# Kernel tuning notes

Hardware: AMD Instinct MI355X
Metric: run time of the kernel (lower is better)

Reference implementation:

```python
import jax, jax.numpy as jnp
import numpy as np


def setup_inputs() -> dict:
    key = jax.random.key(0)
    ks = jax.random.split(key, 8)
    B, C, H, W = 8, 256, 64, 64
    Ck = C // 8
    s = 0.02
    return {
        "x": jax.random.normal(ks[0], (B, C, H, W), dtype=jnp.float32),
        "Wk": jax.random.normal(ks[1], (Ck, C), dtype=jnp.float32) * s,
        "bk": jnp.zeros((Ck,), dtype=jnp.float32),
        "Wq": jax.random.normal(ks[2], (Ck, C), dtype=jnp.float32) * s,
        "bq": jnp.zeros((Ck,), dtype=jnp.float32),
        "Wv": jax.random.normal(ks[3], (C, C), dtype=jnp.float32) * s,
        "bv": jnp.zeros((C,), dtype=jnp.float32),
        "gamma": jnp.zeros((1,), dtype=jnp.float32),
    }


def reference(x, Wk, bk, Wq, bq, Wv, bv, gamma):
    B, C, H, W = x.shape
    x_flat = x.reshape(B, C, H * W)  # [B, C, N]
    # 1x1 conv1d == pointwise linear over channels
    k = jnp.einsum('oc,bcn->bon', Wk, x_flat) + bk[None, :, None]  # [B, C/8, N]
    q = jnp.einsum('oc,bcn->bon', Wq, x_flat) + bq[None, :, None]  # [B, C/8, N]
    v = jnp.einsum('oc,bcn->bon', Wv, x_flat) + bv[None, :, None]  # [B, C, N]
    affinity = jnp.einsum('bki,bkj->bij', q, k)  # [B, N, N]
    # NOTE: original computes F.softmax(affinity, dim=1) but never uses it
    # (dead code); output uses the raw affinity, reproduced faithfully here.
    out = jnp.einsum('bci,bih->bch', v, affinity).reshape(B, C, H, W)
    return gamma[0] * out + x
```

## Files before the change

### kernel.cpp

```cpp
#include <hip/hip_runtime.h>


constexpr int NB = 8;
constexpr int NC = 256;
constexpr int NK = 32;
constexpr int NN = 4096;
constexpr int NCHUNK = 64;

typedef float  f32x4  __attribute__((ext_vector_type(4)));
typedef __bf16 bf16x4 __attribute__((ext_vector_type(4)));
typedef __bf16 bf16x8 __attribute__((ext_vector_type(8)));

__device__ __forceinline__ bf16x8 load_bf8(const float* __restrict__ p) {
  f32x4 a = *(const f32x4*)p;
  f32x4 b = *(const f32x4*)(p + 4);
  bf16x8 r;
  r[0] = (__bf16)a[0]; r[1] = (__bf16)a[1]; r[2] = (__bf16)a[2]; r[3] = (__bf16)a[3];
  r[4] = (__bf16)b[0]; r[5] = (__bf16)b[1]; r[6] = (__bf16)b[2]; r[7] = (__bf16)b[3];
  return r;
}

__global__ __launch_bounds__(256) void k_front(
    const float* __restrict__ x, const float* __restrict__ Wq,
    const float* __restrict__ bq, const float* __restrict__ Wk,
    __bf16* __restrict__ Tpart, __bf16* __restrict__ Kt_t,
    float* __restrict__ qsum_part) {
  __shared__ __bf16 ldsT[64 * 264];
  __shared__ __bf16 ldsW[2][32][264];
  __shared__ __bf16 ldsQt[32][72];
  __shared__ __bf16 ldsKt[32][72];
  __shared__ float  ldsQs[4][32];
  int bid = blockIdx.x;
  int b = bid >> 6, chunk = bid & 63;
  int nsub = chunk * 64;
  int t = threadIdx.x;
  int lane = t & 63, w = t >> 6, lr = lane & 15, lg = lane >> 4;
  const float* xb = x + (size_t)b * NC * NN;
  float bq0 = bq[lr], bq1 = bq[16 + lr];

  {
    int m = t >> 7, tid = t & 127;
    int j = tid >> 2, c0 = (tid & 3) * 64;
    const float* Ws = m ? Wk : Wq;
#pragma unroll
    for (int i = 0; i < 16; ++i) {
      f32x4 v = *(const f32x4*)(Ws + j * NC + c0 + i * 4);
      bf16x4 pk = {(__bf16)v[0], (__bf16)v[1], (__bf16)v[2], (__bf16)v[3]};
      *(bf16x4*)&ldsW[m][j][c0 + i * 4] = pk;
    }
  }
  {
    int cg = t >> 4, ng = t & 15;
    int n0 = ng * 4;
    int swzEl = (ng & 7) << 3;
#pragma unroll
    for (int r = 0; r < 4; ++r) {
      int c0 = r * 64 + cg * 4;
      const float* src = xb + (size_t)c0 * NN + nsub + n0;
      f32x4 L0 = *(const f32x4*)(src);
      f32x4 L1 = *(const f32x4*)(src + NN);
      f32x4 L2 = *(const f32x4*)(src + 2 * NN);
      f32x4 L3 = *(const f32x4*)(src + 3 * NN);
#pragma unroll
      for (int jj = 0; jj < 4; ++jj) {
        bf16x4 pk = {(__bf16)L0[jj], (__bf16)L1[jj], (__bf16)L2[jj], (__bf16)L3[jj]};
        *(bf16x4*)&ldsT[(n0 + jj) * 264 + (c0 ^ swzEl)] = pk;
      }
    }
  }
  __syncthreads();
  f32x4 aq[2] = {}, ak[2] = {};
  {
    int n = w * 16 + lr;
    int swzA = ((n >> 2) & 7) << 3;
    int rowA = n * 264;
#pragma unroll
    for (int ks = 0; ks < 8; ++ks) {
      bf16x8 af = *(const bf16x8*)&ldsT[rowA + ((ks * 32 + lg * 8) ^ swzA)];
      bf16x8 q0 = *(const bf16x8*)&ldsW[0][lr][ks * 32 + lg * 8];
      bf16x8 q1 = *(const bf16x8*)&ldsW[0][16 + lr][ks * 32 + lg * 8];
      bf16x8 k0 = *(const bf16x8*)&ldsW[1][lr][ks * 32 + lg * 8];
      bf16x8 k1 = *(const bf16x8*)&ldsW[1][16 + lr][ks * 32 + lg * 8];
      aq[0] = __builtin_amdgcn_mfma_f32_16x16x32_bf16(af, q0, aq[0], 0, 0, 0);
      aq[1] = __builtin_amdgcn_mfma_f32_16x16x32_bf16(af, q1, aq[1], 0, 0, 0);
      ak[0] = __builtin_amdgcn_mfma_f32_16x16x32_bf16(af, k0, ak[0], 0, 0, 0);
      ak[1] = __builtin_amdgcn_mfma_f32_16x16x32_bf16(af, k1, ak[1], 0, 0, 0);
    }
  }
  float qs0, qs1;
#pragma unroll
  for (int r = 0; r < 4; ++r) { aq[0][r] += bq0; aq[1][r] += bq1; }
  qs0 = aq[0][0] + aq[0][1] + aq[0][2] + aq[0][3];
  qs1 = aq[1][0] + aq[1][1] + aq[1][2] + aq[1][3];
  {
    bf16x4 p0 = {(__bf16)aq[0][0], (__bf16)aq[0][1], (__bf16)aq[0][2], (__bf16)aq[0][3]};
    bf16x4 p1 = {(__bf16)aq[1][0], (__bf16)aq[1][1], (__bf16)aq[1][2], (__bf16)aq[1][3]};
    *(bf16x4*)&ldsQt[lr][w * 16 + lg * 4] = p0;
    *(bf16x4*)&ldsQt[16 + lr][w * 16 + lg * 4] = p1;
    bf16x4 k0p = {(__bf16)ak[0][0], (__bf16)ak[0][1], (__bf16)ak[0][2], (__bf16)ak[0][3]};
    bf16x4 k1p = {(__bf16)ak[1][0], (__bf16)ak[1][1], (__bf16)ak[1][2], (__bf16)ak[1][3]};
    *(bf16x4*)&ldsKt[lr][w * 16 + lg * 4] = k0p;
    *(bf16x4*)&ldsKt[16 + lr][w * 16 + lg * 4] = k1p;
  }
  __syncthreads();
  {
    int nloc = t >> 2, j0 = (t & 3) * 8;
    bf16x8 pk;
#pragma unroll
    for (int i = 0; i < 8; ++i) pk[i] = ldsKt[j0 + i][nloc];
    *(bf16x8*)&Kt_t[((size_t)b * NN + nsub + nloc) * NK + j0] = pk;
  }
  f32x4 accT[4][2] = {};
#pragma unroll
  for (int ks2 = 0; ks2 < 2; ++ks2) {
    bf16x8 bf0 = *(const bf16x8*)&ldsQt[lr][ks2 * 32 + lg * 8];
    bf16x8 bf1 = *(const bf16x8*)&ldsQt[16 + lr][ks2 * 32 + lg * 8];
#pragma unroll
    for (int mt = 0; mt < 4; ++mt) {
      int c = w * 64 + mt * 16 + lr;
      bf16x8 af = load_bf8(xb + (size_t)c * NN + nsub + ks2 * 32 + lg * 8);
      accT[mt][0] = __builtin_amdgcn_mfma_f32_16x16x32_bf16(af, bf0, accT[mt][0], 0, 0, 0);
      accT[mt][1] = __builtin_amdgcn_mfma_f32_16x16x32_bf16(af, bf1, accT[mt][1], 0, 0, 0);
    }
  }
  qs0 += __shfl_xor(qs0, 16); qs0 += __shfl_xor(qs0, 32);
  qs1 += __shfl_xor(qs1, 16); qs1 += __shfl_xor(qs1, 32);
  if (lane < 16) { ldsQs[w][lane] = qs0; ldsQs[w][16 + lane] = qs1; }
  __syncthreads();
  if (t < 32)
    qsum_part[(size_t)(chunk * NB + b) * NK + t] =
        ldsQs[0][t] + ldsQs[1][t] + ldsQs[2][t] + ldsQs[3][t];
  __bf16* Tp = Tpart + (size_t)(chunk * NB + b) * NC * NK;
#pragma unroll
  for (int mt = 0; mt < 4; ++mt)
#pragma unroll
    for (int jf = 0; jf < 2; ++jf) {
      bf16x4 pk = {(__bf16)accT[mt][jf][0], (__bf16)accT[mt][jf][1],
                   (__bf16)accT[mt][jf][2], (__bf16)accT[mt][jf][3]};
      *(bf16x4*)&Tp[(jf * 16 + lr) * NC + w * 64 + mt * 16 + lg * 4] = pk;
    }
}

__global__ __launch_bounds__(256) void k_reduce(__bf16* __restrict__ Tpart) {
  int bid = blockIdx.x;
  int b = bid >> 3, slice = bid & 7;
  int t = threadIdx.x;
  int jo = t >> 6, c0 = (t & 63) * 4;
  const size_t chstride = (size_t)NB * NK * NC;
  size_t idx = ((size_t)b * NK + slice * 4 + jo) * NC + c0;
  float acc[4] = {};
#pragma unroll 8
  for (int ch = 0; ch < NCHUNK; ++ch) {
    bf16x4 v = *(const bf16x4*)&Tpart[ch * chstride + idx];
#pragma unroll
    for (int i = 0; i < 4; ++i) acc[i] += (float)v[i];
  }
  bf16x4 o = {(__bf16)acc[0], (__bf16)acc[1], (__bf16)acc[2], (__bf16)acc[3]};
  *(bf16x4*)&Tpart[idx] = o;
}

__global__ __launch_bounds__(256) void k_pgemm(
    const __bf16* __restrict__ T, const float* __restrict__ qsum_part,
    const float* __restrict__ Wv, const float* __restrict__ bv,
    const float* __restrict__ bk, __bf16* __restrict__ P,
    float* __restrict__ h2) {
  __shared__ __bf16 shTt[16][264];
  __shared__ float shQsum[16];
  int bid = blockIdx.x;
  int b = bid >> 1, jg = bid & 1;
  int t = threadIdx.x;
  if (t < 16) {
    float s = 0.f;
#pragma unroll 8
    for (int ch = 0; ch < NCHUNK; ++ch)
      s += qsum_part[(size_t)(ch * NB + b) * NK + jg * 16 + t];
    shQsum[t] = s;
  }
  {
    int j = t >> 5, c0 = (t & 31) * 8;
    bf16x8 v = *(const bf16x8*)&T[((size_t)b * NK + jg * 16 + j) * NC + c0];
    *(bf16x8*)&shTt[j][c0] = v;
  }
  __syncthreads();
  int lane = t & 63, w = t >> 6, lr = lane & 15, lg = lane >> 4;
  float bkj = bk[jg * 16 + lr];
  f32x4 accP[4] = {};
#pragma unroll
  for (int ks = 0; ks < 8; ++ks) {
    bf16x8 b0 = *(const bf16x8*)&shTt[lr][ks * 32 + lg * 8];
#pragma unroll
    for (int mt = 0; mt < 4; ++mt) {
      int c = w * 64 + mt * 16 + lr;
      bf16x8 af = load_bf8(Wv + (size_t)c * NC + ks * 32 + lg * 8);
      accP[mt] = __builtin_amdgcn_mfma_f32_16x16x32_bf16(af, b0, accP[mt], 0, 0, 0);
    }
  }
  float qs = shQsum[lr];
#pragma unroll
  for (int mt = 0; mt < 4; ++mt) {
    float hacc[4];
#pragma unroll
    for (int r = 0; r < 4; ++r) {
      int c = w * 64 + mt * 16 + lg * 4 + r;
      float val = accP[mt][r] + bv[c] * qs;
      P[((size_t)b * NC + c) * NK + jg * 16 + lr] = (__bf16)val;
      hacc[r] = val * bkj;
    }
#pragma unroll
    for (int r = 0; r < 4; ++r) {
      float v = hacc[r];
      v += __shfl_xor(v, 1); v += __shfl_xor(v, 2);
      v += __shfl_xor(v, 4); v += __shfl_xor(v, 8);
      if (lr == 0)
        h2[((size_t)b * 2 + jg) * NC + w * 64 + mt * 16 + lg * 4 + r] = v;
    }
  }
}

__global__ __launch_bounds__(256) void k_back(
    const float* __restrict__ x, const __bf16* __restrict__ Kt_t,
    const __bf16* __restrict__ P, const float* __restrict__ h2,
    const float* __restrict__ gamma, float* __restrict__ out) {
  int bid = blockIdx.x;
  int b = bid >> 6, n0 = (bid & 63) * 64;
  int t = threadIdx.x;
  int lane = t & 63, w = t >> 6, lr = lane & 15, lg = lane >> 4;

  bf16x8 af = *(const bf16x8*)&Kt_t[((size_t)b * NN + n0 + w * 16 + lr) * NK + lg * 8];
  const __bf16* Pb = P + (size_t)b * NC * NK;
  f32x4 acc[16];
#pragma unroll
  for (int ft = 0; ft < 16; ++ft) {
    bf16x8 bfr = *(const bf16x8*)&Pb[(size_t)(ft * 16 + lr) * NK + lg * 8];
    f32x4 z = {0.f, 0.f, 0.f, 0.f};
    acc[ft] = __builtin_amdgcn_mfma_f32_16x16x32_bf16(af, bfr, z, 0, 0, 0);
  }
  float g = gamma[0];
  const float* h0 = h2 + (size_t)b * 2 * NC;
#pragma unroll
  for (int ft = 0; ft < 16; ++ft) {
    int c = ft * 16 + lr;
    float hc = h0[c] + h0[NC + c];
    size_t idx = ((size_t)b * NC + c) * NN + n0 + w * 16 + lg * 4;
    f32x4 xv = *(const f32x4*)&x[idx];
    f32x4 o;
#pragma unroll
    for (int r = 0; r < 4; ++r) o[r] = g * (acc[ft][r] + hc) + xv[r];
    *(f32x4*)&out[idx] = o;
  }
}

extern "C" void kernel_launch(void* const* d_in, const int* in_sizes, int n_in,
                              void* d_out, int out_size, void* d_ws, size_t ws_size,
                              hipStream_t stream) {
  (void)in_sizes; (void)n_in; (void)out_size; (void)ws_size;
  const float* x     = (const float*)d_in[0];
  const float* Wk    = (const float*)d_in[1];
  const float* bk    = (const float*)d_in[2];
  const float* Wq    = (const float*)d_in[3];
  const float* bq    = (const float*)d_in[4];
  const float* Wv    = (const float*)d_in[5];
  const float* bv    = (const float*)d_in[6];
  const float* gamma = (const float*)d_in[7];
  float* out = (float*)d_out;

  char* wsb = (char*)d_ws;
  const size_t tpB = (size_t)NCHUNK * NB * NC * NK * 2;
  const size_t ktB = (size_t)NB * NN * NK * 2;
  const size_t qsB = (size_t)NCHUNK * NB * NK * 4;
  const size_t pB  = (size_t)NB * NC * NK * 2;
  __bf16* Tpart = (__bf16*)wsb;
  __bf16* Kt_t  = (__bf16*)(wsb + tpB);
  float*  qsp   = (float*)(wsb + tpB + ktB);
  __bf16* P     = (__bf16*)(wsb + tpB + ktB + qsB);
  float*  h2    = (float*)(wsb + tpB + ktB + qsB + pB);

  k_front<<<NB * NCHUNK, 256, 0, stream>>>(x, Wq, bq, Wk, Tpart, Kt_t, qsp);
  k_reduce<<<NB * 8, 256, 0, stream>>>(Tpart);
  k_pgemm<<<NB * 2, 256, 0, stream>>>(Tpart, qsp, Wv, bv, bk, P, h2);
  k_back<<<NB * 64, 256, 0, stream>>>(x, Kt_t, P, h2, gamma, out);
}
```

Baseline: 52.17 us.

## Halve front-kernel chunk size, split Q/K across waves, two-level T reduction

Doubles the number of front-kernel blocks by processing 32 columns per block instead of 64. Q and K projections move to separate wave pairs, with weights read straight from global memory instead of staged in LDS. The T-partial reduction becomes two-level: 4x more reduce blocks produce quarter sums, and k_pgemm adds the four quarters. The aim is higher occupancy and parallelism in the front and reduce stages, at the cost of twice the Tpart partial traffic and redundant weight loads per wave.

```diff
diff --git a/kernel.cpp b/kernel.cpp
--- a/kernel.cpp
+++ b/kernel.cpp
@@ -5,7 +5,7 @@
 constexpr int NC = 256;
 constexpr int NK = 32;
 constexpr int NN = 4096;
-constexpr int NCHUNK = 64;
+constexpr int NCHUNK = 128;
 
 typedef float  f32x4  __attribute__((ext_vector_type(4)));
 typedef __bf16 bf16x4 __attribute__((ext_vector_type(4)));
@@ -25,37 +25,27 @@
     const float* __restrict__ bq, const float* __restrict__ Wk,
     __bf16* __restrict__ Tpart, __bf16* __restrict__ Kt_t,
     float* __restrict__ qsum_part) {
-  __shared__ __bf16 ldsT[64 * 264];
-  __shared__ __bf16 ldsW[2][32][264];
-  __shared__ __bf16 ldsQt[32][72];
-  __shared__ __bf16 ldsKt[32][72];
-  __shared__ float  ldsQs[4][32];
-  int bid = blockIdx.x;
-  int b = bid >> 6, chunk = bid & 63;
-  int nsub = chunk * 64;
+  __shared__ __bf16 ldsT[32 * 264];
+  __shared__ __bf16 ldsQt[32][36];
+  __shared__ __bf16 ldsKt[32][36];
+  __shared__ float  ldsQs[2][32];
+  int bid = blockIdx.x;
+  int b = bid >> 7, chunk = bid & 127;
+  int nsub = chunk * 32;
   int t = threadIdx.x;
   int lane = t & 63, w = t >> 6, lr = lane & 15, lg = lane >> 4;
   const float* xb = x + (size_t)b * NC * NN;
+  const bool isQ = (w < 2);
+  const float* Wrow = isQ ? Wq : Wk;
   float bq0 = bq[lr], bq1 = bq[16 + lr];
 
   {
-    int m = t >> 7, tid = t & 127;
-    int j = tid >> 2, c0 = (tid & 3) * 64;
-    const float* Ws = m ? Wk : Wq;
-#pragma unroll
-    for (int i = 0; i < 16; ++i) {
-      f32x4 v = *(const f32x4*)(Ws + j * NC + c0 + i * 4);
-      bf16x4 pk = {(__bf16)v[0], (__bf16)v[1], (__bf16)v[2], (__bf16)v[3]};
-      *(bf16x4*)&ldsW[m][j][c0 + i * 4] = pk;
-    }
-  }
-  {
-    int cg = t >> 4, ng = t & 15;
+    int ng = t & 7, cg = t >> 3;
     int n0 = ng * 4;
-    int swzEl = (ng & 7) << 3;
-#pragma unroll
-    for (int r = 0; r < 4; ++r) {
-      int c0 = r * 64 + cg * 4;
+    int swzEl = ng << 3;
+#pragma unroll
+    for (int r = 0; r < 2; ++r) {
+      int c0 = cg * 8 + r * 4;
       const float* src = xb + (size_t)c0 * NN + nsub + n0;
       f32x4 L0 = *(const f32x4*)(src);
       f32x4 L1 = *(const f32x4*)(src + NN);
@@ -69,41 +59,44 @@
     }
   }
   __syncthreads();
-  f32x4 aq[2] = {}, ak[2] = {};
-  {
-    int n = w * 16 + lr;
+  f32x4 a0 = {}, a1 = {};
+  {
+    int n = (w & 1) * 16 + lr;
     int swzA = ((n >> 2) & 7) << 3;
     int rowA = n * 264;
 #pragma unroll
     for (int ks = 0; ks < 8; ++ks) {
       bf16x8 af = *(const bf16x8*)&ldsT[rowA + ((ks * 32 + lg * 8) ^ swzA)];
-      bf16x8 q0 = *(const bf16x8*)&ldsW[0][lr][ks * 32 + lg * 8];
-      bf16x8 q1 = *(const bf16x8*)&ldsW[0][16 + lr][ks * 32 + lg * 8];
-      bf16x8 k0 = *(const bf16x8*)&ldsW[1][lr][ks * 32 + lg * 8];
-      bf16x8 k1 = *(const bf16x8*)&ldsW[1][16 + lr][ks * 32 + lg * 8];
-      aq[0] = __builtin_amdgcn_mfma_f32_16x16x32_bf16(af, q0, aq[0], 0, 0, 0);
-      aq[1] = __builtin_amdgcn_mfma_f32_16x16x32_bf16(af, q1, aq[1], 0, 0, 0);
-      ak[0] = __builtin_amdgcn_mfma_f32_16x16x32_bf16(af, k0, ak[0], 0, 0, 0);
-      ak[1] = __builtin_amdgcn_mfma_f32_16x16x32_bf16(af, k1, ak[1], 0, 0, 0);
-    }
-  }
-  float qs0, qs1;
-#pragma unroll
-  for (int r = 0; r < 4; ++r) { aq[0][r] += bq0; aq[1][r] += bq1; }
-  qs0 = aq[0][0] + aq[0][1] + aq[0][2] + aq[0][3];
-  qs1 = aq[1][0] + aq[1][1] + aq[1][2] + aq[1][3];
-  {
-    bf16x4 p0 = {(__bf16)aq[0][0], (__bf16)aq[0][1], (__bf16)aq[0][2], (__bf16)aq[0][3]};
-    bf16x4 p1 = {(__bf16)aq[1][0], (__bf16)aq[1][1], (__bf16)aq[1][2], (__bf16)aq[1][3]};
-    *(bf16x4*)&ldsQt[lr][w * 16 + lg * 4] = p0;
-    *(bf16x4*)&ldsQt[16 + lr][w * 16 + lg * 4] = p1;
-    bf16x4 k0p = {(__bf16)ak[0][0], (__bf16)ak[0][1], (__bf16)ak[0][2], (__bf16)ak[0][3]};
-    bf16x4 k1p = {(__bf16)ak[1][0], (__bf16)ak[1][1], (__bf16)ak[1][2], (__bf16)ak[1][3]};
-    *(bf16x4*)&ldsKt[lr][w * 16 + lg * 4] = k0p;
-    *(bf16x4*)&ldsKt[16 + lr][w * 16 + lg * 4] = k1p;
+      bf16x8 w0 = load_bf8(Wrow + (size_t)lr * NC + ks * 32 + lg * 8);
+      bf16x8 w1 = load_bf8(Wrow + (size_t)(16 + lr) * NC + ks * 32 + lg * 8);
+      a0 = __builtin_amdgcn_mfma_f32_16x16x32_bf16(af, w0, a0, 0, 0, 0);
+      a1 = __builtin_amdgcn_mfma_f32_16x16x32_bf16(af, w1, a1, 0, 0, 0);
+    }
+  }
+  if (isQ) {
+#pragma unroll
+    for (int r = 0; r < 4; ++r) { a0[r] += bq0; a1[r] += bq1; }
+    float qs0 = a0[0] + a0[1] + a0[2] + a0[3];
+    float qs1 = a1[0] + a1[1] + a1[2] + a1[3];
+    bf16x4 p0 = {(__bf16)a0[0], (__bf16)a0[1], (__bf16)a0[2], (__bf16)a0[3]};
+    bf16x4 p1 = {(__bf16)a1[0], (__bf16)a1[1], (__bf16)a1[2], (__bf16)a1[3]};
+    int nq = (w & 1) * 16 + lg * 4;
+    *(bf16x4*)&ldsQt[lr][nq] = p0;
+    *(bf16x4*)&ldsQt[16 + lr][nq] = p1;
+    qs0 += __shfl_xor(qs0, 16); qs0 += __shfl_xor(qs0, 32);
+    qs1 += __shfl_xor(qs1, 16); qs1 += __shfl_xor(qs1, 32);
+    if (lane < 16) { ldsQs[w][lane] = qs0; ldsQs[w][16 + lane] = qs1; }
+  } else {
+    bf16x4 p0 = {(__bf16)a0[0], (__bf16)a0[1], (__bf16)a0[2], (__bf16)a0[3]};
+    bf16x4 p1 = {(__bf16)a1[0], (__bf16)a1[1], (__bf16)a1[2], (__bf16)a1[3]};
+    int nq = (w & 1) * 16 + lg * 4;
+    *(bf16x4*)&ldsKt[lr][nq] = p0;
+    *(bf16x4*)&ldsKt[16 + lr][nq] = p1;
   }
   __syncthreads();
-  {
+  if (t < 32)
+    qsum_part[(size_t)(chunk * NB + b) * NK + t] = ldsQs[0][t] + ldsQs[1][t];
+  if (t < 128) {
     int nloc = t >> 2, j0 = (t & 3) * 8;
     bf16x8 pk;
 #pragma unroll
@@ -111,25 +104,17 @@
     *(bf16x8*)&Kt_t[((size_t)b * NN + nsub + nloc) * NK + j0] = pk;
   }
   f32x4 accT[4][2] = {};
-#pragma unroll
-  for (int ks2 = 0; ks2 < 2; ++ks2) {
-    bf16x8 bf0 = *(const bf16x8*)&ldsQt[lr][ks2 * 32 + lg * 8];
-    bf16x8 bf1 = *(const bf16x8*)&ldsQt[16 + lr][ks2 * 32 + lg * 8];
+  {
+    bf16x8 bf0 = *(const bf16x8*)&ldsQt[lr][lg * 8];
+    bf16x8 bf1 = *(const bf16x8*)&ldsQt[16 + lr][lg * 8];
 #pragma unroll
     for (int mt = 0; mt < 4; ++mt) {
       int c = w * 64 + mt * 16 + lr;
-      bf16x8 af = load_bf8(xb + (size_t)c * NN + nsub + ks2 * 32 + lg * 8);
+      bf16x8 af = load_bf8(xb + (size_t)c * NN + nsub + lg * 8);
       accT[mt][0] = __builtin_amdgcn_mfma_f32_16x16x32_bf16(af, bf0, accT[mt][0], 0, 0, 0);
       accT[mt][1] = __builtin_amdgcn_mfma_f32_16x16x32_bf16(af, bf1, accT[mt][1], 0, 0, 0);
     }
   }
-  qs0 += __shfl_xor(qs0, 16); qs0 += __shfl_xor(qs0, 32);
-  qs1 += __shfl_xor(qs1, 16); qs1 += __shfl_xor(qs1, 32);
-  if (lane < 16) { ldsQs[w][lane] = qs0; ldsQs[w][16 + lane] = qs1; }
-  __syncthreads();
-  if (t < 32)
-    qsum_part[(size_t)(chunk * NB + b) * NK + t] =
-        ldsQs[0][t] + ldsQs[1][t] + ldsQs[2][t] + ldsQs[3][t];
   __bf16* Tp = Tpart + (size_t)(chunk * NB + b) * NC * NK;
 #pragma unroll
   for (int mt = 0; mt < 4; ++mt)
@@ -141,26 +126,29 @@
     }
 }
 
-__global__ __launch_bounds__(256) void k_reduce(__bf16* __restrict__ Tpart) {
-  int bid = blockIdx.x;
-  int b = bid >> 3, slice = bid & 7;
+__global__ __launch_bounds__(256) void k_reduce(
+    const __bf16* __restrict__ Tpart, __bf16* __restrict__ Tq) {
+  int bid = blockIdx.x;
+  int b = bid >> 5, r = bid & 31;
+  int js = r >> 2, cq = r & 3;
   int t = threadIdx.x;
   int jo = t >> 6, c0 = (t & 63) * 4;
   const size_t chstride = (size_t)NB * NK * NC;
-  size_t idx = ((size_t)b * NK + slice * 4 + jo) * NC + c0;
+  size_t idx = ((size_t)b * NK + js * 4 + jo) * NC + c0;
+  const __bf16* src = Tpart + (size_t)(cq * 32) * chstride + idx;
   float acc[4] = {};
 #pragma unroll 8
-  for (int ch = 0; ch < NCHUNK; ++ch) {
-    bf16x4 v = *(const bf16x4*)&Tpart[ch * chstride + idx];
+  for (int ch = 0; ch < 32; ++ch) {
+    bf16x4 v = *(const bf16x4*)&src[ch * chstride];
 #pragma unroll
     for (int i = 0; i < 4; ++i) acc[i] += (float)v[i];
   }
   bf16x4 o = {(__bf16)acc[0], (__bf16)acc[1], (__bf16)acc[2], (__bf16)acc[3]};
-  *(bf16x4*)&Tpart[idx] = o;
+  *(bf16x4*)&Tq[((size_t)(cq * NB + b) * NK + js * 4 + jo) * NC + c0] = o;
 }
 
 __global__ __launch_bounds__(256) void k_pgemm(
-    const __bf16* __restrict__ T, const float* __restrict__ qsum_part,
+    const __bf16* __restrict__ Tq, const float* __restrict__ qsum_part,
     const float* __restrict__ Wv, const float* __restrict__ bv,
     const float* __restrict__ bk, __bf16* __restrict__ P,
     float* __restrict__ h2) {
@@ -177,9 +165,21 @@
     shQsum[t] = s;
   }
   {
-    int j = t >> 5, c0 = (t & 31) * 8;
-    bf16x8 v = *(const bf16x8*)&T[((size_t)b * NK + jg * 16 + j) * NC + c0];
-    *(bf16x8*)&shTt[j][c0] = v;
+    int j = t >> 4, c0 = (t & 15) * 16;
+    float acc[16] = {};
+#pragma unroll
+    for (int cq = 0; cq < 4; ++cq) {
+      const __bf16* src = &Tq[((size_t)(cq * NB + b) * NK + jg * 16 + j) * NC + c0];
+      bf16x8 v0 = *(const bf16x8*)src;
+      bf16x8 v1 = *(const bf16x8*)(src + 8);
+#pragma unroll
+      for (int i = 0; i < 8; ++i) { acc[i] += (float)v0[i]; acc[8 + i] += (float)v1[i]; }
+    }
+    bf16x8 o0, o1;
+#pragma unroll
+    for (int i = 0; i < 8; ++i) { o0[i] = (__bf16)acc[i]; o1[i] = (__bf16)acc[8 + i]; }
+    *(bf16x8*)&shTt[j][c0] = o0;
+    *(bf16x8*)&shTt[j][c0 + 8] = o1;
   }
   __syncthreads();
   int lane = t & 63, w = t >> 6, lr = lane & 15, lg = lane >> 4;
@@ -267,16 +267,18 @@
   char* wsb = (char*)d_ws;
   const size_t tpB = (size_t)NCHUNK * NB * NC * NK * 2;
   const size_t ktB = (size_t)NB * NN * NK * 2;
+  const size_t tqB = (size_t)4 * NB * NC * NK * 2;
   const size_t qsB = (size_t)NCHUNK * NB * NK * 4;
   const size_t pB  = (size_t)NB * NC * NK * 2;
   __bf16* Tpart = (__bf16*)wsb;
   __bf16* Kt_t  = (__bf16*)(wsb + tpB);
-  float*  qsp   = (float*)(wsb + tpB + ktB);
-  __bf16* P     = (__bf16*)(wsb + tpB + ktB + qsB);
-  float*  h2    = (float*)(wsb + tpB + ktB + qsB + pB);
+  __bf16* Tq    = (__bf16*)(wsb + tpB + ktB);
+  float*  qsp   = (float*)(wsb + tpB + ktB + tqB);
+  __bf16* P     = (__bf16*)(wsb + tpB + ktB + tqB + qsB);
+  float*  h2    = (float*)(wsb + tpB + ktB + tqB + qsB + pB);
 
   k_front<<<NB * NCHUNK, 256, 0, stream>>>(x, Wq, bq, Wk, Tpart, Kt_t, qsp);
-  k_reduce<<<NB * 8, 256, 0, stream>>>(Tpart);
-  k_pgemm<<<NB * 2, 256, 0, stream>>>(Tpart, qsp, Wv, bv, bk, P, h2);
+  k_reduce<<<NB * 32, 256, 0, stream>>>(Tpart, Tq);
+  k_pgemm<<<NB * 2, 256, 0, stream>>>(Tq, qsp, Wv, bv, bk, P, h2);
   k_back<<<NB * 64, 256, 0, stream>>>(x, Kt_t, P, h2, gamma, out);
 }
```

Result: slower. 65.38 us (+25.3%).

## Fuse chunk reduction into P-GEMM kernel with finer j-slicing

Applied to the files above, without the earlier changes.

Merges the k_reduce and k_pgemm kernels into one k_mid kernel. Each block reduces its 4 j-rows of the chunk partials straight into shared memory and then runs the Wv MFMA on them, zero-padding the unused 12 MFMA rows. This removes one kernel launch and the bf16 round-trip of the reduced T through global memory. The grid goes from 16 to 64 blocks, and the partial h sums are now written as 8 slices per channel for k_back to add up. In exchange, three quarters of the MFMA work is wasted on padding, and every block reloads Wv.

```diff
diff --git a/kernel.cpp b/kernel.cpp
--- a/kernel.cpp
+++ b/kernel.cpp
@@ -141,53 +141,50 @@
     }
 }
 
-__global__ __launch_bounds__(256) void k_reduce(__bf16* __restrict__ Tpart) {
-  int bid = blockIdx.x;
-  int b = bid >> 3, slice = bid & 7;
-  int t = threadIdx.x;
-  int jo = t >> 6, c0 = (t & 63) * 4;
-  const size_t chstride = (size_t)NB * NK * NC;
-  size_t idx = ((size_t)b * NK + slice * 4 + jo) * NC + c0;
-  float acc[4] = {};
-#pragma unroll 8
-  for (int ch = 0; ch < NCHUNK; ++ch) {
-    bf16x4 v = *(const bf16x4*)&Tpart[ch * chstride + idx];
-#pragma unroll
-    for (int i = 0; i < 4; ++i) acc[i] += (float)v[i];
-  }
-  bf16x4 o = {(__bf16)acc[0], (__bf16)acc[1], (__bf16)acc[2], (__bf16)acc[3]};
-  *(bf16x4*)&Tpart[idx] = o;
-}
-
-__global__ __launch_bounds__(256) void k_pgemm(
-    const __bf16* __restrict__ T, const float* __restrict__ qsum_part,
+__global__ __launch_bounds__(256) void k_mid(
+    const __bf16* __restrict__ Tpart, const float* __restrict__ qsum_part,
     const float* __restrict__ Wv, const float* __restrict__ bv,
     const float* __restrict__ bk, __bf16* __restrict__ P,
-    float* __restrict__ h2) {
-  __shared__ __bf16 shTt[16][264];
-  __shared__ float shQsum[16];
+    float* __restrict__ h8) {
+  __shared__ __bf16 shT[16][264];
+  __shared__ float shQ[4];
   int bid = blockIdx.x;
-  int b = bid >> 1, jg = bid & 1;
+  int b = bid >> 3, js = bid & 7;
   int t = threadIdx.x;
-  if (t < 16) {
+  if (t < 4) {
     float s = 0.f;
 #pragma unroll 8
     for (int ch = 0; ch < NCHUNK; ++ch)
-      s += qsum_part[(size_t)(ch * NB + b) * NK + jg * 16 + t];
-    shQsum[t] = s;
-  }
-  {
-    int j = t >> 5, c0 = (t & 31) * 8;
-    bf16x8 v = *(const bf16x8*)&T[((size_t)b * NK + jg * 16 + j) * NC + c0];
-    *(bf16x8*)&shTt[j][c0] = v;
+      s += qsum_part[(size_t)(ch * NB + b) * NK + js * 4 + t];
+    shQ[t] = s;
+  }
+  if (t < 64 && t >= 4) {
+  }
+  {
+    for (int i = t; i < 12 * 264; i += 256) shT[4 + i / 264][i % 264] = (__bf16)0.f;
+  }
+  {
+    int jo = t >> 6, c0 = (t & 63) * 4;
+    const size_t chstride = (size_t)NB * NK * NC;
+    size_t idx = ((size_t)b * NK + js * 4 + jo) * NC + c0;
+    float acc[4] = {};
+#pragma unroll 8
+    for (int ch = 0; ch < NCHUNK; ++ch) {
+      bf16x4 v = *(const bf16x4*)&Tpart[ch * chstride + idx];
+#pragma unroll
+      for (int i = 0; i < 4; ++i) acc[i] += (float)v[i];
+    }
+    bf16x4 o = {(__bf16)acc[0], (__bf16)acc[1], (__bf16)acc[2], (__bf16)acc[3]};
+    *(bf16x4*)&shT[jo][c0] = o;
   }
   __syncthreads();
   int lane = t & 63, w = t >> 6, lr = lane & 15, lg = lane >> 4;
-  float bkj = bk[jg * 16 + lr];
+  float bkj = bk[js * 4 + (lr & 3)];
+  float qs = shQ[lr & 3];
   f32x4 accP[4] = {};
 #pragma unroll
   for (int ks = 0; ks < 8; ++ks) {
-    bf16x8 b0 = *(const bf16x8*)&shTt[lr][ks * 32 + lg * 8];
+    bf16x8 b0 = *(const bf16x8*)&shT[lr][ks * 32 + lg * 8];
 #pragma unroll
     for (int mt = 0; mt < 4; ++mt) {
       int c = w * 64 + mt * 16 + lr;
@@ -195,7 +192,6 @@
       accP[mt] = __builtin_amdgcn_mfma_f32_16x16x32_bf16(af, b0, accP[mt], 0, 0, 0);
     }
   }
-  float qs = shQsum[lr];
 #pragma unroll
   for (int mt = 0; mt < 4; ++mt) {
     float hacc[4];
@@ -203,23 +199,24 @@
     for (int r = 0; r < 4; ++r) {
       int c = w * 64 + mt * 16 + lg * 4 + r;
       float val = accP[mt][r] + bv[c] * qs;
-      P[((size_t)b * NC + c) * NK + jg * 16 + lr] = (__bf16)val;
+      if (lr < 4) P[((size_t)b * NC + c) * NK + js * 4 + lr] = (__bf16)val;
       hacc[r] = val * bkj;
     }
 #pragma unroll
     for (int r = 0; r < 4; ++r) {
       float v = hacc[r];
       v += __shfl_xor(v, 1); v += __shfl_xor(v, 2);
-      v += __shfl_xor(v, 4); v += __shfl_xor(v, 8);
-      if (lr == 0)
-        h2[((size_t)b * 2 + jg) * NC + w * 64 + mt * 16 + lg * 4 + r] = v;
+      if (lr == 0) {
+        int c = w * 64 + mt * 16 + lg * 4 + r;
+        h8[((size_t)b * NC + c) * 8 + js] = v;
+      }
     }
   }
 }
 
 __global__ __launch_bounds__(256) void k_back(
     const float* __restrict__ x, const __bf16* __restrict__ Kt_t,
-    const __bf16* __restrict__ P, const float* __restrict__ h2,
+    const __bf16* __restrict__ P, const float* __restrict__ h8,
     const float* __restrict__ gamma, float* __restrict__ out) {
   int bid = blockIdx.x;
   int b = bid >> 6, n0 = (bid & 63) * 64;
@@ -236,11 +233,14 @@
     acc[ft] = __builtin_amdgcn_mfma_f32_16x16x32_bf16(af, bfr, z, 0, 0, 0);
   }
   float g = gamma[0];
-  const float* h0 = h2 + (size_t)b * 2 * NC;
+  const float* hb = h8 + (size_t)b * NC * 8;
 #pragma unroll
   for (int ft = 0; ft < 16; ++ft) {
     int c = ft * 16 + lr;
-    float hc = h0[c] + h0[NC + c];
+    f32x4 hv0 = *(const f32x4*)&hb[c * 8];
+    f32x4 hv1 = *(const f32x4*)&hb[c * 8 + 4];
+    float hc = (hv0[0] + hv0[1] + hv0[2] + hv0[3]) +
+               (hv1[0] + hv1[1] + hv1[2] + hv1[3]);
     size_t idx = ((size_t)b * NC + c) * NN + n0 + w * 16 + lg * 4;
     f32x4 xv = *(const f32x4*)&x[idx];
     f32x4 o;
@@ -273,10 +273,9 @@
   __bf16* Kt_t  = (__bf16*)(wsb + tpB);
   float*  qsp   = (float*)(wsb + tpB + ktB);
   __bf16* P     = (__bf16*)(wsb + tpB + ktB + qsB);
-  float*  h2    = (float*)(wsb + tpB + ktB + qsB + pB);
+  float*  h8    = (float*)(wsb + tpB + ktB + qsB + pB);
 
   k_front<<<NB * NCHUNK, 256, 0, stream>>>(x, Wq, bq, Wk, Tpart, Kt_t, qsp);
-  k_reduce<<<NB * 8, 256, 0, stream>>>(Tpart);
-  k_pgemm<<<NB * 2, 256, 0, stream>>>(Tpart, qsp, Wv, bv, bk, P, h2);
-  k_back<<<NB * 64, 256, 0, stream>>>(x, Kt_t, P, h2, gamma, out);
-}
+  k_mid<<<NB * 8, 256, 0, stream>>>(Tpart, qsp, Wv, bv, bk, P, h8);
+  k_back<<<NB * 64, 256, 0, stream>>>(x, Kt_t, P, h8, gamma, out);
+}
```

Result: slower. 54.22 us (+3.9%).

## Split x transpose and bf16 conversion into a separate pre-pass kernel

Applied to the files above, without the earlier changes.

Adds a kernel that reads x once in fp32 and writes two bf16 copies, a channel-major one and a transposed [n][c] one. k_front then reads these from global memory instead of transposing through shared memory and converting fp32 on the fly. The aim is to shrink k_front's LDS footprint and load traffic, which may raise occupancy. The cost is an extra launch and about 32 MB of additional global writes and reads. k_pgemm's T staging loop is also changed to two 16-byte loads per thread.

```diff
diff --git a/kernel.cpp b/kernel.cpp
--- a/kernel.cpp
+++ b/kernel.cpp
@@ -20,12 +20,57 @@
   return r;
 }
 
+__global__ __launch_bounds__(256) void k_xt(
+    const float* __restrict__ x, __bf16* __restrict__ xT,
+    __bf16* __restrict__ xbf) {
+  __shared__ __bf16 tr[64 * 72];
+  int bid = blockIdx.x;
+  int b = bid >> 8, r = bid & 255;
+  int n0 = (r >> 2) * 64, c0t = (r & 3) * 64;
+  int t = threadIdx.x;
+  int cg = t >> 4, ng = t & 15;
+  int crow = c0t + cg * 4;
+  const float* src = x + ((size_t)b * NC + crow) * NN + n0 + ng * 4;
+  f32x4 L0 = *(const f32x4*)(src);
+  f32x4 L1 = *(const f32x4*)(src + NN);
+  f32x4 L2 = *(const f32x4*)(src + 2 * NN);
+  f32x4 L3 = *(const f32x4*)(src + 3 * NN);
+  {
+    __bf16* dst = xbf + ((size_t)b * NC + crow) * NN + n0 + ng * 4;
+    bf16x4 r0 = {(__bf16)L0[0], (__bf16)L0[1], (__bf16)L0[2], (__bf16)L0[3]};
+    bf16x4 r1 = {(__bf16)L1[0], (__bf16)L1[1], (__bf16)L1[2], (__bf16)L1[3]};
+    bf16x4 r2 = {(__bf16)L2[0], (__bf16)L2[1], (__bf16)L2[2], (__bf16)L2[3]};
+    bf16x4 r3 = {(__bf16)L3[0], (__bf16)L3[1], (__bf16)L3[2], (__bf16)L3[3]};
+    *(bf16x4*)(dst) = r0;
+    *(bf16x4*)(dst + NN) = r1;
+    *(bf16x4*)(dst + 2 * NN) = r2;
+    *(bf16x4*)(dst + 3 * NN) = r3;
+  }
+  {
+    int swz = (ng & 7) << 3;
+#pragma unroll
+    for (int jj = 0; jj < 4; ++jj) {
+      bf16x4 pk = {(__bf16)L0[jj], (__bf16)L1[jj], (__bf16)L2[jj], (__bf16)L3[jj]};
+      *(bf16x4*)&tr[(ng * 4 + jj) * 72 + ((cg * 4) ^ swz)] = pk;
+    }
+  }
+  __syncthreads();
+  {
+    int nloc = t >> 2, j0 = (t & 3) * 16;
+    int swzr = ((nloc >> 2) & 7) << 3;
+    bf16x8 v0 = *(const bf16x8*)&tr[nloc * 72 + (j0 ^ swzr)];
+    bf16x8 v1 = *(const bf16x8*)&tr[nloc * 72 + ((j0 + 8) ^ swzr)];
+    __bf16* dst = xT + ((size_t)b * NN + n0 + nloc) * NC + c0t + j0;
+    *(bf16x8*)dst = v0;
+    *(bf16x8*)(dst + 8) = v1;
+  }
+}
+
 __global__ __launch_bounds__(256) void k_front(
-    const float* __restrict__ x, const float* __restrict__ Wq,
-    const float* __restrict__ bq, const float* __restrict__ Wk,
-    __bf16* __restrict__ Tpart, __bf16* __restrict__ Kt_t,
-    float* __restrict__ qsum_part) {
-  __shared__ __bf16 ldsT[64 * 264];
+    const __bf16* __restrict__ xT, const __bf16* __restrict__ xbf,
+    const float* __restrict__ Wq, const float* __restrict__ bq,
+    const float* __restrict__ Wk, __bf16* __restrict__ Tpart,
+    __bf16* __restrict__ Kt_t, float* __restrict__ qsum_part) {
   __shared__ __bf16 ldsW[2][32][264];
   __shared__ __bf16 ldsQt[32][72];
   __shared__ __bf16 ldsKt[32][72];
@@ -35,7 +80,6 @@
   int nsub = chunk * 64;
   int t = threadIdx.x;
   int lane = t & 63, w = t >> 6, lr = lane & 15, lg = lane >> 4;
-  const float* xb = x + (size_t)b * NC * NN;
   float bq0 = bq[lr], bq1 = bq[16 + lr];
 
   {
@@ -49,34 +93,13 @@
       *(bf16x4*)&ldsW[m][j][c0 + i * 4] = pk;
     }
   }
-  {
-    int cg = t >> 4, ng = t & 15;
-    int n0 = ng * 4;
-    int swzEl = (ng & 7) << 3;
-#pragma unroll
-    for (int r = 0; r < 4; ++r) {
-      int c0 = r * 64 + cg * 4;
-      const float* src = xb + (size_t)c0 * NN + nsub + n0;
-      f32x4 L0 = *(const f32x4*)(src);
-      f32x4 L1 = *(const f32x4*)(src + NN);
-      f32x4 L2 = *(const f32x4*)(src + 2 * NN);
-      f32x4 L3 = *(const f32x4*)(src + 3 * NN);
-#pragma unroll
-      for (int jj = 0; jj < 4; ++jj) {
-        bf16x4 pk = {(__bf16)L0[jj], (__bf16)L1[jj], (__bf16)L2[jj], (__bf16)L3[jj]};
-        *(bf16x4*)&ldsT[(n0 + jj) * 264 + (c0 ^ swzEl)] = pk;
-      }
-    }
-  }
   __syncthreads();
   f32x4 aq[2] = {}, ak[2] = {};
   {
-    int n = w * 16 + lr;
-    int swzA = ((n >> 2) & 7) << 3;
-    int rowA = n * 264;
+    const __bf16* xtrow = xT + ((size_t)b * NN + nsub + w * 16 + lr) * NC;
 #pragma unroll
     for (int ks = 0; ks < 8; ++ks) {
-      bf16x8 af = *(const bf16x8*)&ldsT[rowA + ((ks * 32 + lg * 8) ^ swzA)];
+      bf16x8 af = *(const bf16x8*)&xtrow[ks * 32 + lg * 8];
       bf16x8 q0 = *(const bf16x8*)&ldsW[0][lr][ks * 32 + lg * 8];
       bf16x8 q1 = *(const bf16x8*)&ldsW[0][16 + lr][ks * 32 + lg * 8];
       bf16x8 k0 = *(const bf16x8*)&ldsW[1][lr][ks * 32 + lg * 8];
@@ -118,7 +141,7 @@
 #pragma unroll
     for (int mt = 0; mt < 4; ++mt) {
       int c = w * 64 + mt * 16 + lr;
-      bf16x8 af = load_bf8(xb + (size_t)c * NN + nsub + ks2 * 32 + lg * 8);
+      bf16x8 af = *(const bf16x8*)&xbf[((size_t)b * NC + c) * NN + nsub + ks2 * 32 + lg * 8];
       accT[mt][0] = __builtin_amdgcn_mfma_f32_16x16x32_bf16(af, bf0, accT[mt][0], 0, 0, 0);
       accT[mt][1] = __builtin_amdgcn_mfma_f32_16x16x32_bf16(af, bf1, accT[mt][1], 0, 0, 0);
     }
@@ -177,9 +200,12 @@
     shQsum[t] = s;
   }
   {
-    int j = t >> 5, c0 = (t & 31) * 8;
-    bf16x8 v = *(const bf16x8*)&T[((size_t)b * NK + jg * 16 + j) * NC + c0];
-    *(bf16x8*)&shTt[j][c0] = v;
+    int j = t >> 4, c0 = (t & 15) * 16;
+    const __bf16* src = &T[((size_t)b * NK + jg * 16 + j) * NC + c0];
+    bf16x8 v0 = *(const bf16x8*)src;
+    bf16x8 v1 = *(const bf16x8*)(src + 8);
+    *(bf16x8*)&shTt[j][c0] = v0;
+    *(bf16x8*)&shTt[j][c0 + 8] = v1;
   }
   __syncthreads();
   int lane = t & 63, w = t >> 6, lr = lane & 15, lg = lane >> 4;
@@ -265,17 +291,22 @@
   float* out = (float*)d_out;
 
   char* wsb = (char*)d_ws;
+  const size_t xtB = (size_t)NB * NN * NC * 2;
+  const size_t xbB = (size_t)NB * NC * NN * 2;
   const size_t tpB = (size_t)NCHUNK * NB * NC * NK * 2;
   const size_t ktB = (size_t)NB * NN * NK * 2;
   const size_t qsB = (size_t)NCHUNK * NB * NK * 4;
   const size_t pB  = (size_t)NB * NC * NK * 2;
-  __bf16* Tpart = (__bf16*)wsb;
-  __bf16* Kt_t  = (__bf16*)(wsb + tpB);
-  float*  qsp   = (float*)(wsb + tpB + ktB);
-  __bf16* P     = (__bf16*)(wsb + tpB + ktB + qsB);
-  float*  h2    = (float*)(wsb + tpB + ktB + qsB + pB);
-
-  k_front<<<NB * NCHUNK, 256, 0, stream>>>(x, Wq, bq, Wk, Tpart, Kt_t, qsp);
+  __bf16* xT    = (__bf16*)wsb;
+  __bf16* xbf   = (__bf16*)(wsb + xtB);
+  __bf16* Tpart = (__bf16*)(wsb + xtB + xbB);
+  __bf16* Kt_t  = (__bf16*)(wsb + xtB + xbB + tpB);
+  float*  qsp   = (float*)(wsb + xtB + xbB + tpB + ktB);
+  __bf16* P     = (__bf16*)(wsb + xtB + xbB + tpB + ktB + qsB);
+  float*  h2    = (float*)(wsb + xtB + xbB + tpB + ktB + qsB + pB);
+
+  k_xt<<<NB * 64 * 4, 256, 0, stream>>>(x, xT, xbf);
+  k_front<<<NB * NCHUNK, 256, 0, stream>>>(xT, xbf, Wq, bq, Wk, Tpart, Kt_t, qsp);
   k_reduce<<<NB * 8, 256, 0, stream>>>(Tpart);
   k_pgemm<<<NB * 2, 256, 0, stream>>>(Tpart, qsp, Wv, bv, bk, P, h2);
   k_back<<<NB * 64, 256, 0, stream>>>(x, Kt_t, P, h2, gamma, out);
```

Result: slower. 62.35 us (+19.5%).
